# Performance work log

Measured on AMD Instinct MI355X. Metric: run time of the kernel, lower is better.

Reference implementation:

```python
import jax, jax.numpy as jnp
import numpy as np

B, M, C, D, FF, FEAT = 1, 1024, 128, 512, 1024, 20
PAIR = 3 * D + 2 * FEAT  # slow_scorer_size = 1576


def _ffnn(x, W0, b0, W1, b1):
    # FFNN(depth=1): hidden relu layer then linear output (eval mode, no dropout)
    return jax.nn.relu(x @ W0 + b0) @ W1 + b1


def _batch_gather(x, idx):
    # x: [B, M, ...], idx: [B, ...] int -> gather along mention dim per batch
    return jax.vmap(lambda xb, ib: xb[ib])(x, idx)


def _bucket_distance(d):
    # log-scale distance buckets 0..9 (identity for d<=4)
    log_idx = jnp.floor(jnp.log(jnp.maximum(d, 1).astype(jnp.float32)) / jnp.log(2.0)).astype(jnp.int32) + 3
    return jnp.clip(jnp.where(d <= 4, d, log_idx), 0, 9)


def setup_inputs() -> dict:
    key = jax.random.key(0)
    ks = jax.random.split(key, 10)
    s = 0.02
    return {
        'mention_emb': jax.random.normal(ks[0], (B, M, D), dtype=jnp.float32),
        'mention_cluster_ids': jax.random.randint(ks[1], (B, M), 0, 200),
        'mention_speaker_ids': jax.random.randint(ks[2], (B, M), 0, 2),
        'ms_W0': jax.random.normal(ks[3], (D, FF), dtype=jnp.float32) * s,
        'ms_b0': jnp.zeros((FF,), jnp.float32),
        'ms_W1': jax.random.normal(ks[4], (FF, 1), dtype=jnp.float32) * s,
        'ms_b1': jnp.zeros((1,), jnp.float32),
        'sp_W0': jax.random.normal(ks[5], (PAIR, FF), dtype=jnp.float32) * s,
        'sp_b0': jnp.zeros((FF,), jnp.float32),
        'sp_W1': jax.random.normal(ks[6], (FF, 1), dtype=jnp.float32) * s,
        'sp_b1': jnp.zeros((1,), jnp.float32),
        'speaker_emb': jax.random.normal(ks[7], (2, FEAT), dtype=jnp.float32) * s,
        'bucket_emb': jax.random.normal(ks[8], (10, FEAT), dtype=jnp.float32) * s,
    }


def reference(mention_emb, mention_cluster_ids, mention_speaker_ids,
              ms_W0, ms_b0, ms_W1, ms_b1,
              sp_W0, sp_b0, sp_W1, sp_b1,
              speaker_emb, bucket_emb):
    # mention scoring
    mention_scores = _ffnn(mention_emb, ms_W0, ms_b0, ms_W1, ms_b1)[..., 0]  # [B, M]

    # get_antecedent_info: fixed window of C previous mentions
    offsets = jnp.arange(1, C + 1)[None, None, :]                    # [1,1,C]
    raw = jnp.arange(M)[None, :, None] - offsets                      # [1,M,C]
    antecedents = jnp.broadcast_to(jnp.clip(raw, 0, M - 1), (B, M, C))
    ant_mask = jnp.broadcast_to(raw >= 0, (B, M, C))

    fast_scores = _batch_gather(mention_scores, antecedents) + mention_scores[:, :, None]
    antecedent_emb = _batch_gather(mention_emb, antecedents)          # [B,M,C,D]

    # slow pair scorer features
    same_speaker = (_batch_gather(mention_speaker_ids, antecedents) == mention_speaker_ids[:, :, None]).astype(jnp.int32)
    speaker_feat = speaker_emb[same_speaker]                          # [B,M,C,FEAT]
    bucket_feat = jnp.broadcast_to(bucket_emb[_bucket_distance(offsets)], (B, M, C, FEAT))

    src = jnp.broadcast_to(mention_emb[:, :, None, :], (B, M, C, D))
    pair_emb = jnp.concatenate([src, antecedent_emb, src * antecedent_emb, speaker_feat, bucket_feat], axis=-1)
    slow_scores = _ffnn(pair_emb, sp_W0, sp_b0, sp_W1, sp_b1)[..., 0]  # [B,M,C]

    antecedent_scores = fast_scores + slow_scores + jnp.log(ant_mask.astype(jnp.float32))
    overall_scores = jnp.concatenate([jnp.zeros((B, M, 1), jnp.float32), antecedent_scores], axis=2)
    overall_dist = jax.nn.softmax(overall_scores, axis=-1)
    eps = 1e-6
    overall_dist = jnp.clip(overall_dist, eps, 1.0 - eps)
    overall_dist = overall_dist / jnp.sum(overall_dist, axis=-1, keepdims=True)

    # coref loss from cluster ids
    ant_cluster = _batch_gather(mention_cluster_ids, antecedents) * ant_mask.astype(mention_cluster_ids.dtype)
    same_cluster = ant_cluster == mention_cluster_ids[:, :, None]
    non_dummy = (mention_cluster_ids > 0)[:, :, None]
    ant_labels = same_cluster & non_dummy
    dummy_labels = ~jnp.any(ant_labels, axis=2, keepdims=True)
    overall_labels = jnp.concatenate([dummy_labels, ant_labels], axis=2)
    loss = -jnp.sum(jnp.log(overall_dist) * overall_labels.astype(jnp.float32), axis=2)
    loss = jnp.mean(jnp.sum(loss, axis=1))
    return overall_dist, loss
```

## Files before the change

kernel.cpp:

```cpp
#include <hip/hip_runtime.h>
#include <math.h>

#define MM 1024
#define DD 512
#define CC 128
#define LDSR 516


typedef __attribute__((ext_vector_type(8))) short bf16x8;
typedef __attribute__((ext_vector_type(4), aligned(8))) short bf16x4a;
typedef __attribute__((ext_vector_type(4))) float f32x4;

__device__ __forceinline__ ushort bf16_rn(float x) {
    uint u = __float_as_uint(x);
    uint r = u + 0x7fffu + ((u >> 16) & 1u);
    return (ushort)(r >> 16);
}
__device__ __forceinline__ float bf16_to_f(ushort u) {
    return __uint_as_float(((uint)u) << 16);
}
__device__ __forceinline__ bf16x8 ld_lds16(const ushort* p) {
    bf16x4a lo = *(const bf16x4a*)p;
    bf16x4a hi = *(const bf16x4a*)(p + 4);
    return __builtin_shufflevector(lo, hi, 0, 1, 2, 3, 4, 5, 6, 7);
}

__global__ __launch_bounds__(256) void prep_all(
    const float* __restrict__ emb, ushort* __restrict__ embb,
    const float* __restrict__ ms_W0, const float* __restrict__ sp_W0,
    ushort* __restrict__ Wall, ushort* __restrict__ WfragP,
    const float* __restrict__ speaker_emb, const float* __restrict__ bucket_emb,
    float* __restrict__ spk_proj, float* __restrict__ bkt_proj)
{
    const int bid = blockIdx.x;
    const int tid = threadIdx.x;

    if (bid < 1024) {
        int i = bid * 256 + tid;
        float2 v = ((const float2*)emb)[i];
        ushort2 o;
        o.x = bf16_rn(v.x);
        o.y = bf16_rn(v.y);
        ((ushort2*)embb)[i] = o;
        return;
    }
    if (bid < 1408) {
        __shared__ float t[64][65];
        const int r = bid - 1024;
        const int k0 = (r & 7) * 64;
        const int n0 = (r >> 3) * 64;
        const int g = n0 >> 10;
        const float* src = (g == 0) ? ms_W0 : (sp_W0 + (size_t)(g - 1) * 512 * 1024);
        const int col0 = n0 & 1023;
        const int tr = tid >> 6, tc = tid & 63;
#pragma unroll
        for (int i = 0; i < 16; ++i) {
            int k = tr + i * 4;
            t[k][tc] = src[(size_t)(k0 + k) * 1024 + col0 + tc];
        }
        __syncthreads();
        const int f = tid >> 2;
        const int c4 = tid & 3;
        ushort tmp[16];
#pragma unroll
        for (int j = 0; j < 16; ++j) tmp[j] = bf16_rn(t[c4 * 16 + j][f]);
        uint4* dst = (uint4*)(Wall + (size_t)(n0 + f) * 512 + k0 + c4 * 16);
        dst[0] = *(uint4*)&tmp[0];
        dst[1] = *(uint4*)&tmp[8];
        return;
    }
    if (bid < 1664) {
        const int b4 = (bid - 1408) * 4 + (tid >> 6);
        const int l = tid & 63;
        const int g2 = b4 >> 5, s = (b4 >> 1) & 15, j = b4 & 1;
        const int wv = g2 >> 2, ft = g2 & 3;
        const int t16 = wv * 8 + ft * 2 + j;
        const int f = t16 * 16 + (l & 15);
        const int kb = s * 32 + ((l >> 4) & 3) * 8;
        const float* W = sp_W0 + (size_t)1024 * 1024;
        ushort tmp[8];
#pragma unroll
        for (int e = 0; e < 8; ++e) tmp[e] = bf16_rn(W[(size_t)(kb + e) * 1024 + f]);
        uint4* dst = (uint4*)(WfragP + (size_t)b4 * 512 + l * 8);
        *dst = *(uint4*)&tmp[0];
        return;
    }
    {
        const int r = bid - 1664;
        const float* e; const float* W; float* out;
        if (r < 2) { e = speaker_emb + r * 20; W = sp_W0 + (size_t)1536 * 1024; out = spk_proj + r * 1024; }
        else       { e = bucket_emb + (r - 2) * 20; W = sp_W0 + (size_t)1556 * 1024; out = bkt_proj + (r - 2) * 1024; }
        float ek[20];
#pragma unroll
        for (int k = 0; k < 20; ++k) ek[k] = e[k];
        for (int f = tid; f < 1024; f += 256) {
            float s = 0.f;
#pragma unroll
            for (int k = 0; k < 20; ++k) s = fmaf(ek[k], W[(size_t)k * 1024 + f], s);
            out[f] = s;
        }
        return;
    }
}

__global__ __launch_bounds__(256) void gemm_h_ms(
    const ushort* __restrict__ embb, const ushort* __restrict__ Wall,
    const float* __restrict__ ms_b0, const float* __restrict__ ms_W1,
    float* __restrict__ H, float* __restrict__ ms)
{
    const int n0 = blockIdx.x * 128;
    const int m0 = blockIdx.y * 128;
    const int lane = threadIdx.x & 63, wave = threadIdx.x >> 6;
    const int wx = wave & 1, wy = wave >> 1;
    const int l15 = lane & 15, lq = lane >> 4;

    const ushort* arow[4];
#pragma unroll
    for (int mi = 0; mi < 4; ++mi)
        arow[mi] = embb + (size_t)(m0 + wy * 64 + mi * 16 + l15) * 512;
    const ushort* brow[4];
#pragma unroll
    for (int ni = 0; ni < 4; ++ni)
        brow[ni] = Wall + (size_t)(n0 + wx * 64 + ni * 16 + l15) * 512;

    f32x4 acc[4][4];
#pragma unroll
    for (int i = 0; i < 4; ++i)
#pragma unroll
        for (int j = 0; j < 4; ++j) acc[i][j] = (f32x4)0.f;

    for (int kt = 0; kt < 512; kt += 32) {
        const int ko = kt + lq * 8;
        bf16x8 av[4], bv[4];
#pragma unroll
        for (int mi = 0; mi < 4; ++mi) av[mi] = *(const bf16x8*)(arow[mi] + ko);
#pragma unroll
        for (int ni = 0; ni < 4; ++ni) bv[ni] = *(const bf16x8*)(brow[ni] + ko);
#pragma unroll
        for (int mi = 0; mi < 4; ++mi)
#pragma unroll
            for (int ni = 0; ni < 4; ++ni)
                acc[mi][ni] = __builtin_amdgcn_mfma_f32_16x16x32_bf16(av[mi], bv[ni], acc[mi][ni], 0, 0, 0);
    }

    if (n0 < 1024) {
        float b0v[4], w1v[4];
#pragma unroll
        for (int ni = 0; ni < 4; ++ni) {
            const int col = n0 + wx * 64 + ni * 16 + l15;
            b0v[ni] = ms_b0[col];
            w1v[ni] = ms_W1[col];
        }
#pragma unroll
        for (int mi = 0; mi < 4; ++mi)
#pragma unroll
            for (int r = 0; r < 4; ++r) {
                float s = 0.f;
#pragma unroll
                for (int ni = 0; ni < 4; ++ni)
                    s += fmaxf(acc[mi][ni][r] + b0v[ni], 0.f) * w1v[ni];
                s += __shfl_xor(s, 1); s += __shfl_xor(s, 2);
                s += __shfl_xor(s, 4); s += __shfl_xor(s, 8);
                if (l15 == 0) {
                    const int mrow = m0 + wy * 64 + mi * 16 + lq * 4 + r;
                    atomicAdd(&ms[mrow], s);
                }
            }
    } else {
#pragma unroll
        for (int mi = 0; mi < 4; ++mi)
#pragma unroll
            for (int r = 0; r < 4; ++r) {
                int mrow = m0 + wy * 64 + mi * 16 + lq * 4 + r;
#pragma unroll
                for (int ni = 0; ni < 4; ++ni)
                    H[(size_t)mrow * 3072 + n0 + wx * 64 + ni * 16 + l15] = acc[mi][ni][r];
            }
    }
}

__global__ __launch_bounds__(512, 8) void pair_mfma(
    const ushort* __restrict__ embb, const ushort* __restrict__ WfragP,
    const float* __restrict__ H, const float* __restrict__ spk_proj,
    const float* __restrict__ bkt_proj, const float* __restrict__ sp_b0,
    const float* __restrict__ sp_W1, const int* __restrict__ speaker,
    float* __restrict__ slow)
{
    extern __shared__ ushort Alds[];
    float* red = (float*)(Alds + 32 * LDSR);
    int* meta_ss = (int*)(red + 8 * 32);
    int* meta_bk = meta_ss + 32;
    const int m = blockIdx.x;
    const int cq = blockIdx.y;
    const int cbase = cq * 32;
    const int tid = threadIdx.x;
    const int spk_m = speaker[m];

    {
        const int c = tid & 31;
        const int kh = (tid >> 5) * 32;
        int a = m - 1 - (cbase + c); if (a < 0) a = 0;
        const ushort* ea = embb + (size_t)a * 512 + kh;
        const ushort* em = embb + (size_t)m * 512 + kh;
        ushort* dst = Alds + c * LDSR + kh;
#pragma unroll
        for (int j = 0; j < 32; j += 8) {
            bf16x8 va = *(const bf16x8*)(ea + j);
            bf16x8 vm = *(const bf16x8*)(em + j);
            uint pr[4];
#pragma unroll
            for (int p = 0; p < 4; ++p) {
                float q0 = bf16_to_f((ushort)va[2 * p])     * bf16_to_f((ushort)vm[2 * p]);
                float q1 = bf16_to_f((ushort)va[2 * p + 1]) * bf16_to_f((ushort)vm[2 * p + 1]);
                pr[p] = __builtin_amdgcn_perm(__float_as_uint(q1), __float_as_uint(q0), 0x07060302u);
            }
            *(uint2*)(dst + j)     = *(uint2*)&pr[0];
            *(uint2*)(dst + j + 4) = *(uint2*)&pr[2];
        }
        if (tid < 32) {
            meta_ss[c] = (speaker[a] == spk_m) ? 1 : 0;
            int off = cbase + c + 1;
            int bk;
            if (off <= 4) bk = off;
            else { bk = 31 - __clz(off) + 3; if (bk > 9) bk = 9; }
            meta_bk[c] = bk;
        }
    }
    __syncthreads();

    const int lane = tid & 63;
    const int wave = __builtin_amdgcn_readfirstlane(tid >> 6);
    const int l15 = lane & 15, lq = lane >> 4;
    const ushort* ab0 = Alds + l15 * LDSR + lq * 8;

    const float* Hsrc = H + m * 3072 + 1024;
    const float* Hant = H + 2048;

    float sacc[2][4];
#pragma unroll
    for (int ct = 0; ct < 2; ++ct)
#pragma unroll
        for (int r = 0; r < 4; ++r) sacc[ct][r] = 0.f;

#pragma unroll 1
    for (int ft = 0; ft < 4; ++ft) {
        const int f0a = wave * 128 + ft * 32;
        const ushort* bb = WfragP + (size_t)(wave * 4 + ft) * 16384 + (size_t)lane * 8;
        f32x4 acc[2][2];
#pragma unroll
        for (int i = 0; i < 2; ++i)
#pragma unroll
            for (int j = 0; j < 2; ++j) acc[i][j] = (f32x4)0.f;

#pragma unroll 4
        for (int s = 0; s < 16; ++s) {
            bf16x8 b0 = *(const bf16x8*)(bb + s * 1024);
            bf16x8 b1 = *(const bf16x8*)(bb + s * 1024 + 512);
            bf16x8 a0 = ld_lds16(ab0 + s * 32);
            bf16x8 a1 = ld_lds16(ab0 + 16 * LDSR + s * 32);
            __builtin_amdgcn_s_setprio(1);
            acc[0][0] = __builtin_amdgcn_mfma_f32_16x16x32_bf16(a0, b0, acc[0][0], 0, 0, 0);
            acc[0][1] = __builtin_amdgcn_mfma_f32_16x16x32_bf16(a0, b1, acc[0][1], 0, 0, 0);
            acc[1][0] = __builtin_amdgcn_mfma_f32_16x16x32_bf16(a1, b0, acc[1][0], 0, 0, 0);
            acc[1][1] = __builtin_amdgcn_mfma_f32_16x16x32_bf16(a1, b1, acc[1][1], 0, 0, 0);
            __builtin_amdgcn_s_setprio(0);
        }

        float srcb[2], w1v[2], sp0v[2], sp1v[2];
#pragma unroll
        for (int fi = 0; fi < 2; ++fi) {
            const int fcol = f0a + fi * 16 + l15;
            srcb[fi] = Hsrc[fcol] + sp_b0[fcol];
            w1v[fi]  = sp_W1[fcol];
            sp0v[fi] = spk_proj[fcol];
            sp1v[fi] = spk_proj[1024 + fcol];
        }
#pragma unroll
        for (int ct = 0; ct < 2; ++ct) {
#pragma unroll
            for (int reg = 0; reg < 4; ++reg) {
                const int cl = ct * 16 + lq * 4 + reg;
                int a = m - 1 - (cbase + cl); if (a < 0) a = 0;
                const int ss = meta_ss[cl];
                const int aidx = a * 3072;
                const int bidx = meta_bk[cl] << 10;
                float s = sacc[ct][reg];
#pragma unroll
                for (int fi = 0; fi < 2; ++fi) {
                    const int fcol = f0a + fi * 16 + l15;
                    float bval = bkt_proj[bidx + fcol];
                    float pre = acc[ct][fi][reg] + srcb[fi] + Hant[aidx + fcol]
                              + (ss ? sp1v[fi] : sp0v[fi]) + bval;
                    s += fmaxf(pre, 0.f) * w1v[fi];
                }
                sacc[ct][reg] = s;
            }
        }
    }

#pragma unroll
    for (int ct = 0; ct < 2; ++ct) {
#pragma unroll
        for (int reg = 0; reg < 4; ++reg) {
            float s = sacc[ct][reg];
            s += __shfl_xor(s, 1); s += __shfl_xor(s, 2);
            s += __shfl_xor(s, 4); s += __shfl_xor(s, 8);
            if (l15 == 0) red[wave * 32 + ct * 16 + lq * 4 + reg] = s;
        }
    }
    __syncthreads();
    if (tid < 32) {
        float s = 0.f;
#pragma unroll
        for (int i = 0; i < 8; ++i) s += red[i * 32 + tid];
        slow[m * 128 + cbase + tid] = s;
    }
}

__device__ __forceinline__ float bsum2(float v, float* sm) {
#pragma unroll
    for (int o = 1; o < 64; o <<= 1) v += __shfl_xor(v, o);
    __syncthreads();
    if ((threadIdx.x & 63) == 0) sm[threadIdx.x >> 6] = v;
    __syncthreads();
    return sm[0] + sm[1];
}
__device__ __forceinline__ float bmax2(float v, float* sm) {
#pragma unroll
    for (int o = 1; o < 64; o <<= 1) v = fmaxf(v, __shfl_xor(v, o));
    __syncthreads();
    if ((threadIdx.x & 63) == 0) sm[threadIdx.x >> 6] = v;
    __syncthreads();
    return fmaxf(sm[0], sm[1]);
}

__global__ __launch_bounds__(128) void softmax_loss(
    const float* __restrict__ slow, const float* __restrict__ ms,
    const float* __restrict__ ms_b1,
    const float* __restrict__ sp_b1, const int* __restrict__ cluster,
    float* __restrict__ out, float* __restrict__ loss_partial)
{
    const int m = blockIdx.x, c = threadIdx.x;
    __shared__ float sm[2];
    const int raw = m - 1 - c;
    const bool maskv = raw >= 0;
    const int a = maskv ? raw : 0;
    float score = slow[(size_t)m * 128 + c] + sp_b1[0]
                + ms[m] + ms[a] + 2.f * ms_b1[0];
    if (!maskv) score = -INFINITY;

    float mx = fmaxf(bmax2(score, sm), 0.f);
    float e = expf(score - mx);
    float e0 = expf(0.f - mx);
    float sum = bsum2(e, sm) + e0;
    float p = e / sum, p0 = e0 / sum;
    const float eps = 1e-6f;
    p  = fminf(fmaxf(p,  eps), 1.f - eps);
    p0 = fminf(fmaxf(p0, eps), 1.f - eps);
    float sum2 = bsum2(p, sm) + p0;
    p /= sum2; p0 /= sum2;
    out[(size_t)m * 129 + 1 + c] = p;
    if (c == 0) out[(size_t)m * 129] = p0;

    const int cid = cluster[m];
    const bool lbl = maskv && (cid > 0) && (cluster[a] == cid);
    float anyc = bsum2(lbl ? 1.f : 0.f, sm);
    float lsum = bsum2(lbl ? -logf(p) : 0.f, sm);
    if (c == 0) {
        if (anyc == 0.f) lsum += -logf(p0);
        loss_partial[m] = lsum;
    }
}

__global__ void loss_sum(const float* __restrict__ lp, float* __restrict__ out) {
    float v = 0.f;
    for (int i = threadIdx.x; i < 1024; i += 256) v += lp[i];
#pragma unroll
    for (int o = 1; o < 64; o <<= 1) v += __shfl_xor(v, o);
    __shared__ float sm[4];
    if ((threadIdx.x & 63) == 0) sm[threadIdx.x >> 6] = v;
    __syncthreads();
    if (threadIdx.x == 0) out[(size_t)1024 * 129] = sm[0] + sm[1] + sm[2] + sm[3];
}

extern "C" void kernel_launch(void* const* d_in, const int* in_sizes, int n_in,
                              void* d_out, int out_size, void* d_ws, size_t ws_size,
                              hipStream_t stream)
{
    const float* emb   = (const float*)d_in[0];
    const int*   clus  = (const int*)  d_in[1];
    const int*   spk   = (const int*)  d_in[2];
    const float* ms_W0 = (const float*)d_in[3];
    const float* ms_b0 = (const float*)d_in[4];
    const float* ms_W1 = (const float*)d_in[5];
    const float* ms_b1 = (const float*)d_in[6];
    const float* sp_W0 = (const float*)d_in[7];
    const float* sp_b0 = (const float*)d_in[8];
    const float* sp_W1 = (const float*)d_in[9];
    const float* sp_b1 = (const float*)d_in[10];
    const float* spke  = (const float*)d_in[11];
    const float* bkte  = (const float*)d_in[12];

    float* ws = (float*)d_ws;
    float* H        = ws;
    float* slow     = ws + 3145728;
    float* spk_proj = ws + 3276800;
    float* bkt_proj = ws + 3278848;
    float* msc      = ws + 3289088;
    float* lossp    = ws + 3290112;
    ushort* embb    = (ushort*)(ws + 3291136);
    ushort* Wall    = (ushort*)(ws + 3553280);
    ushort* WfragP  = Wall + (size_t)3072 * 512;
    float* out = (float*)d_out;

    const int pair_lds = 32 * LDSR * 2 + 8 * 32 * 4 + 2 * 32 * 4;

    static bool attr_set = false;
    if (!attr_set) {
        hipFuncSetAttribute((const void*)&pair_mfma,
                            hipFuncAttributeMaxDynamicSharedMemorySize,
                            pair_lds);
        attr_set = true;
    }

    hipMemsetAsync(msc, 0, 1024 * sizeof(float), stream);
    hipLaunchKernelGGL(prep_all, dim3(1676), dim3(256), 0, stream,
                       emb, embb, ms_W0, sp_W0, Wall, WfragP,
                       spke, bkte, spk_proj, bkt_proj);
    hipLaunchKernelGGL(gemm_h_ms, dim3(24, 8), dim3(256), 0, stream,
                       embb, Wall, ms_b0, ms_W1, H, msc);
    hipLaunchKernelGGL(pair_mfma, dim3(1024, 4), dim3(512), pair_lds, stream,
                       embb, WfragP, H, spk_proj, bkt_proj, sp_b0, sp_W1, spk, slow);
    hipLaunchKernelGGL(softmax_loss, dim3(1024), dim3(128), 0, stream,
                       slow, msc, ms_b1, sp_b1, clus, out, lossp);
    hipLaunchKernelGGL(loss_sum, dim3(1), dim3(256), 0, stream, lossp, out);
}
```

Before: 329.2 us.

## Use 32x32x16 MFMA in pair kernel, shrink gemm tiles, fold memset into prep

The pair kernel now uses a single 32x32x16 bf16 MFMA per k-step instead of four 16x16x32 MFMAs, with a new weight fragment layout produced in prep and a restructured epilogue that precomputes antecedent offsets and bucket indices in LDS. The H/mention-score GEMM moves to 64x64 tiles, giving four times as many blocks to fill more CUs. The separate memset of mention scores is folded into the prep kernel, removing one launch. The aim is fewer MFMA and LDS issue slots and better occupancy, at the cost of more per-element epilogue reads and more atomics in the GEMM.

```diff
diff --git a/kernel.cpp b/kernel.cpp
--- a/kernel.cpp
+++ b/kernel.cpp
@@ -10,6 +10,7 @@
 typedef __attribute__((ext_vector_type(8))) short bf16x8;
 typedef __attribute__((ext_vector_type(4), aligned(8))) short bf16x4a;
 typedef __attribute__((ext_vector_type(4))) float f32x4;
+typedef __attribute__((ext_vector_type(16))) float f32x16;
 
 __device__ __forceinline__ ushort bf16_rn(float x) {
     uint u = __float_as_uint(x);
@@ -28,9 +29,10 @@
 __global__ __launch_bounds__(256) void prep_all(
     const float* __restrict__ emb, ushort* __restrict__ embb,
     const float* __restrict__ ms_W0, const float* __restrict__ sp_W0,
-    ushort* __restrict__ Wall, ushort* __restrict__ WfragP,
+    ushort* __restrict__ Wall, ushort* __restrict__ WfragB,
     const float* __restrict__ speaker_emb, const float* __restrict__ bucket_emb,
-    float* __restrict__ spk_proj, float* __restrict__ bkt_proj)
+    float* __restrict__ spk_proj, float* __restrict__ bkt_proj,
+    float* __restrict__ msc)
 {
     const int bid = blockIdx.x;
     const int tid = threadIdx.x;
@@ -70,23 +72,24 @@
         return;
     }
     if (bid < 1664) {
-        const int b4 = (bid - 1408) * 4 + (tid >> 6);
+        const int ts = (bid - 1408) * 4 + (tid >> 6);
         const int l = tid & 63;
-        const int g2 = b4 >> 5, s = (b4 >> 1) & 15, j = b4 & 1;
-        const int wv = g2 >> 2, ft = g2 & 3;
-        const int t16 = wv * 8 + ft * 2 + j;
-        const int f = t16 * 16 + (l & 15);
-        const int kb = s * 32 + ((l >> 4) & 3) * 8;
+        const int tt = ts >> 5, s = ts & 31;
+        const int f = tt * 32 + (l & 31);
+        const int kb = s * 16 + (l >> 5) * 8;
         const float* W = sp_W0 + (size_t)1024 * 1024;
         ushort tmp[8];
 #pragma unroll
         for (int e = 0; e < 8; ++e) tmp[e] = bf16_rn(W[(size_t)(kb + e) * 1024 + f]);
-        uint4* dst = (uint4*)(WfragP + (size_t)b4 * 512 + l * 8);
+        uint4* dst = (uint4*)(WfragB + (size_t)ts * 512 + l * 8);
         *dst = *(uint4*)&tmp[0];
         return;
     }
     {
         const int r = bid - 1664;
+        if (r == 0) {
+            for (int i = tid; i < 1024; i += 256) msc[i] = 0.f;
+        }
         const float* e; const float* W; float* out;
         if (r < 2) { e = speaker_emb + r * 20; W = sp_W0 + (size_t)1536 * 1024; out = spk_proj + r * 1024; }
         else       { e = bucket_emb + (r - 2) * 20; W = sp_W0 + (size_t)1556 * 1024; out = bkt_proj + (r - 2) * 1024; }
@@ -108,79 +111,79 @@
     const float* __restrict__ ms_b0, const float* __restrict__ ms_W1,
     float* __restrict__ H, float* __restrict__ ms)
 {
-    const int n0 = blockIdx.x * 128;
-    const int m0 = blockIdx.y * 128;
+    const int n0 = blockIdx.x * 64;
+    const int m0 = blockIdx.y * 64;
     const int lane = threadIdx.x & 63, wave = threadIdx.x >> 6;
     const int wx = wave & 1, wy = wave >> 1;
     const int l15 = lane & 15, lq = lane >> 4;
 
-    const ushort* arow[4];
-#pragma unroll
-    for (int mi = 0; mi < 4; ++mi)
-        arow[mi] = embb + (size_t)(m0 + wy * 64 + mi * 16 + l15) * 512;
-    const ushort* brow[4];
-#pragma unroll
-    for (int ni = 0; ni < 4; ++ni)
-        brow[ni] = Wall + (size_t)(n0 + wx * 64 + ni * 16 + l15) * 512;
-
-    f32x4 acc[4][4];
-#pragma unroll
-    for (int i = 0; i < 4; ++i)
-#pragma unroll
-        for (int j = 0; j < 4; ++j) acc[i][j] = (f32x4)0.f;
+    const ushort* arow[2];
+#pragma unroll
+    for (int mi = 0; mi < 2; ++mi)
+        arow[mi] = embb + (size_t)(m0 + wy * 32 + mi * 16 + l15) * 512;
+    const ushort* brow[2];
+#pragma unroll
+    for (int ni = 0; ni < 2; ++ni)
+        brow[ni] = Wall + (size_t)(n0 + wx * 32 + ni * 16 + l15) * 512;
+
+    f32x4 acc[2][2];
+#pragma unroll
+    for (int i = 0; i < 2; ++i)
+#pragma unroll
+        for (int j = 0; j < 2; ++j) acc[i][j] = (f32x4)0.f;
 
     for (int kt = 0; kt < 512; kt += 32) {
         const int ko = kt + lq * 8;
-        bf16x8 av[4], bv[4];
-#pragma unroll
-        for (int mi = 0; mi < 4; ++mi) av[mi] = *(const bf16x8*)(arow[mi] + ko);
-#pragma unroll
-        for (int ni = 0; ni < 4; ++ni) bv[ni] = *(const bf16x8*)(brow[ni] + ko);
-#pragma unroll
-        for (int mi = 0; mi < 4; ++mi)
-#pragma unroll
-            for (int ni = 0; ni < 4; ++ni)
+        bf16x8 av[2], bv[2];
+#pragma unroll
+        for (int mi = 0; mi < 2; ++mi) av[mi] = *(const bf16x8*)(arow[mi] + ko);
+#pragma unroll
+        for (int ni = 0; ni < 2; ++ni) bv[ni] = *(const bf16x8*)(brow[ni] + ko);
+#pragma unroll
+        for (int mi = 0; mi < 2; ++mi)
+#pragma unroll
+            for (int ni = 0; ni < 2; ++ni)
                 acc[mi][ni] = __builtin_amdgcn_mfma_f32_16x16x32_bf16(av[mi], bv[ni], acc[mi][ni], 0, 0, 0);
     }
 
     if (n0 < 1024) {
-        float b0v[4], w1v[4];
-#pragma unroll
-        for (int ni = 0; ni < 4; ++ni) {
-            const int col = n0 + wx * 64 + ni * 16 + l15;
+        float b0v[2], w1v[2];
+#pragma unroll
+        for (int ni = 0; ni < 2; ++ni) {
+            const int col = n0 + wx * 32 + ni * 16 + l15;
             b0v[ni] = ms_b0[col];
             w1v[ni] = ms_W1[col];
         }
 #pragma unroll
-        for (int mi = 0; mi < 4; ++mi)
+        for (int mi = 0; mi < 2; ++mi)
 #pragma unroll
             for (int r = 0; r < 4; ++r) {
                 float s = 0.f;
 #pragma unroll
-                for (int ni = 0; ni < 4; ++ni)
+                for (int ni = 0; ni < 2; ++ni)
                     s += fmaxf(acc[mi][ni][r] + b0v[ni], 0.f) * w1v[ni];
                 s += __shfl_xor(s, 1); s += __shfl_xor(s, 2);
                 s += __shfl_xor(s, 4); s += __shfl_xor(s, 8);
                 if (l15 == 0) {
-                    const int mrow = m0 + wy * 64 + mi * 16 + lq * 4 + r;
+                    const int mrow = m0 + wy * 32 + mi * 16 + lq * 4 + r;
                     atomicAdd(&ms[mrow], s);
                 }
             }
     } else {
 #pragma unroll
-        for (int mi = 0; mi < 4; ++mi)
+        for (int mi = 0; mi < 2; ++mi)
 #pragma unroll
             for (int r = 0; r < 4; ++r) {
-                int mrow = m0 + wy * 64 + mi * 16 + lq * 4 + r;
-#pragma unroll
-                for (int ni = 0; ni < 4; ++ni)
-                    H[(size_t)mrow * 3072 + n0 + wx * 64 + ni * 16 + l15] = acc[mi][ni][r];
+                int mrow = m0 + wy * 32 + mi * 16 + lq * 4 + r;
+#pragma unroll
+                for (int ni = 0; ni < 2; ++ni)
+                    H[(size_t)mrow * 3072 + n0 + wx * 32 + ni * 16 + l15] = acc[mi][ni][r];
             }
     }
 }
 
 __global__ __launch_bounds__(512, 8) void pair_mfma(
-    const ushort* __restrict__ embb, const ushort* __restrict__ WfragP,
+    const ushort* __restrict__ embb, const ushort* __restrict__ WfragB,
     const float* __restrict__ H, const float* __restrict__ spk_proj,
     const float* __restrict__ bkt_proj, const float* __restrict__ sp_b0,
     const float* __restrict__ sp_W1, const int* __restrict__ speaker,
@@ -188,8 +191,9 @@
 {
     extern __shared__ ushort Alds[];
     float* red = (float*)(Alds + 32 * LDSR);
-    int* meta_ss = (int*)(red + 8 * 32);
-    int* meta_bk = meta_ss + 32;
+    int* meta_ai = (int*)(red + 8 * 32);
+    int* meta_sb = meta_ai + 32;
+    int* meta_bi = meta_sb + 32;
     const int m = blockIdx.x;
     const int cq = blockIdx.y;
     const int cbase = cq * 32;
@@ -218,95 +222,64 @@
             *(uint2*)(dst + j + 4) = *(uint2*)&pr[2];
         }
         if (tid < 32) {
-            meta_ss[c] = (speaker[a] == spk_m) ? 1 : 0;
+            meta_sb[c] = (speaker[a] == spk_m) ? 1 : 0;
+            meta_ai[c] = a * 3072;
             int off = cbase + c + 1;
             int bk;
             if (off <= 4) bk = off;
             else { bk = 31 - __clz(off) + 3; if (bk > 9) bk = 9; }
-            meta_bk[c] = bk;
+            meta_bi[c] = bk << 10;
         }
     }
     __syncthreads();
 
     const int lane = tid & 63;
     const int wave = __builtin_amdgcn_readfirstlane(tid >> 6);
-    const int l15 = lane & 15, lq = lane >> 4;
-    const ushort* ab0 = Alds + l15 * LDSR + lq * 8;
+    const int l31 = lane & 31, k5 = lane >> 5;
+    const ushort* ab0 = Alds + l31 * LDSR + k5 * 8;
 
     const float* Hsrc = H + m * 3072 + 1024;
     const float* Hant = H + 2048;
 
-    float sacc[2][4];
-#pragma unroll
-    for (int ct = 0; ct < 2; ++ct)
-#pragma unroll
-        for (int r = 0; r < 4; ++r) sacc[ct][r] = 0.f;
+    float sacc[16];
+#pragma unroll
+    for (int r = 0; r < 16; ++r) sacc[r] = 0.f;
 
 #pragma unroll 1
     for (int ft = 0; ft < 4; ++ft) {
-        const int f0a = wave * 128 + ft * 32;
-        const ushort* bb = WfragP + (size_t)(wave * 4 + ft) * 16384 + (size_t)lane * 8;
-        f32x4 acc[2][2];
-#pragma unroll
-        for (int i = 0; i < 2; ++i)
-#pragma unroll
-            for (int j = 0; j < 2; ++j) acc[i][j] = (f32x4)0.f;
+        const ushort* bb = WfragB + (size_t)(wave * 4 + ft) * 16384 + (size_t)lane * 8;
+        f32x16 acc = (f32x16)0.f;
 
 #pragma unroll 4
-        for (int s = 0; s < 16; ++s) {
-            bf16x8 b0 = *(const bf16x8*)(bb + s * 1024);
-            bf16x8 b1 = *(const bf16x8*)(bb + s * 1024 + 512);
-            bf16x8 a0 = ld_lds16(ab0 + s * 32);
-            bf16x8 a1 = ld_lds16(ab0 + 16 * LDSR + s * 32);
+        for (int s = 0; s < 32; ++s) {
+            bf16x8 b = *(const bf16x8*)(bb + s * 512);
+            bf16x8 a = ld_lds16(ab0 + s * 16);
             __builtin_amdgcn_s_setprio(1);
-            acc[0][0] = __builtin_amdgcn_mfma_f32_16x16x32_bf16(a0, b0, acc[0][0], 0, 0, 0);
-            acc[0][1] = __builtin_amdgcn_mfma_f32_16x16x32_bf16(a0, b1, acc[0][1], 0, 0, 0);
-            acc[1][0] = __builtin_amdgcn_mfma_f32_16x16x32_bf16(a1, b0, acc[1][0], 0, 0, 0);
-            acc[1][1] = __builtin_amdgcn_mfma_f32_16x16x32_bf16(a1, b1, acc[1][1], 0, 0, 0);
+            acc = __builtin_amdgcn_mfma_f32_32x32x16_bf16(a, b, acc, 0, 0, 0);
             __builtin_amdgcn_s_setprio(0);
         }
 
-        float srcb[2], w1v[2], sp0v[2], sp1v[2];
-#pragma unroll
-        for (int fi = 0; fi < 2; ++fi) {
-            const int fcol = f0a + fi * 16 + l15;
-            srcb[fi] = Hsrc[fcol] + sp_b0[fcol];
-            w1v[fi]  = sp_W1[fcol];
-            sp0v[fi] = spk_proj[fcol];
-            sp1v[fi] = spk_proj[1024 + fcol];
-        }
-#pragma unroll
-        for (int ct = 0; ct < 2; ++ct) {
-#pragma unroll
-            for (int reg = 0; reg < 4; ++reg) {
-                const int cl = ct * 16 + lq * 4 + reg;
-                int a = m - 1 - (cbase + cl); if (a < 0) a = 0;
-                const int ss = meta_ss[cl];
-                const int aidx = a * 3072;
-                const int bidx = meta_bk[cl] << 10;
-                float s = sacc[ct][reg];
-#pragma unroll
-                for (int fi = 0; fi < 2; ++fi) {
-                    const int fcol = f0a + fi * 16 + l15;
-                    float bval = bkt_proj[bidx + fcol];
-                    float pre = acc[ct][fi][reg] + srcb[fi] + Hant[aidx + fcol]
-                              + (ss ? sp1v[fi] : sp0v[fi]) + bval;
-                    s += fmaxf(pre, 0.f) * w1v[fi];
-                }
-                sacc[ct][reg] = s;
-            }
-        }
-    }
-
-#pragma unroll
-    for (int ct = 0; ct < 2; ++ct) {
-#pragma unroll
-        for (int reg = 0; reg < 4; ++reg) {
-            float s = sacc[ct][reg];
-            s += __shfl_xor(s, 1); s += __shfl_xor(s, 2);
-            s += __shfl_xor(s, 4); s += __shfl_xor(s, 8);
-            if (l15 == 0) red[wave * 32 + ct * 16 + lq * 4 + reg] = s;
-        }
+        const int fcol = wave * 128 + ft * 32 + l31;
+        const float srcb = Hsrc[fcol] + sp_b0[fcol];
+        const float w1v  = sp_W1[fcol];
+        const float sp0  = spk_proj[fcol] + srcb;
+        const float sp1  = spk_proj[1024 + fcol] + srcb;
+#pragma unroll
+        for (int reg = 0; reg < 16; ++reg) {
+            const int cl = (reg & 3) + 8 * (reg >> 2) + 4 * k5;
+            const float spsel = meta_sb[cl] ? sp1 : sp0;
+            float pre = acc[reg] + spsel + Hant[meta_ai[cl] + fcol]
+                      + bkt_proj[meta_bi[cl] + fcol];
+            sacc[reg] += fmaxf(pre, 0.f) * w1v;
+        }
+    }
+
+#pragma unroll
+    for (int reg = 0; reg < 16; ++reg) {
+        float s = sacc[reg];
+        s += __shfl_xor(s, 1); s += __shfl_xor(s, 2);
+        s += __shfl_xor(s, 4); s += __shfl_xor(s, 8); s += __shfl_xor(s, 16);
+        if (l31 == 0) red[wave * 32 + (reg & 3) + 8 * (reg >> 2) + 4 * k5] = s;
     }
     __syncthreads();
     if (tid < 32) {
@@ -410,10 +383,10 @@
     float* lossp    = ws + 3290112;
     ushort* embb    = (ushort*)(ws + 3291136);
     ushort* Wall    = (ushort*)(ws + 3553280);
-    ushort* WfragP  = Wall + (size_t)3072 * 512;
+    ushort* WfragB  = Wall + (size_t)3072 * 512;
     float* out = (float*)d_out;
 
-    const int pair_lds = 32 * LDSR * 2 + 8 * 32 * 4 + 2 * 32 * 4;
+    const int pair_lds = 32 * LDSR * 2 + 8 * 32 * 4 + 3 * 32 * 4;
 
     static bool attr_set = false;
     if (!attr_set) {
@@ -423,14 +396,13 @@
         attr_set = true;
     }
 
-    hipMemsetAsync(msc, 0, 1024 * sizeof(float), stream);
     hipLaunchKernelGGL(prep_all, dim3(1676), dim3(256), 0, stream,
-                       emb, embb, ms_W0, sp_W0, Wall, WfragP,
-                       spke, bkte, spk_proj, bkt_proj);
-    hipLaunchKernelGGL(gemm_h_ms, dim3(24, 8), dim3(256), 0, stream,
+                       emb, embb, ms_W0, sp_W0, Wall, WfragB,
+                       spke, bkte, spk_proj, bkt_proj, msc);
+    hipLaunchKernelGGL(gemm_h_ms, dim3(48, 16), dim3(256), 0, stream,
                        embb, Wall, ms_b0, ms_W1, H, msc);
     hipLaunchKernelGGL(pair_mfma, dim3(1024, 4), dim3(512), pair_lds, stream,
-                       embb, WfragP, H, spk_proj, bkt_proj, sp_b0, sp_W1, spk, slow);
+                       embb, WfragB, H, spk_proj, bkt_proj, sp_b0, sp_W1, spk, slow);
     hipLaunchKernelGGL(softmax_loss, dim3(1024), dim3(128), 0, stream,
                        slow, msc, ms_b1, sp_b1, clus, out, lossp);
     hipLaunchKernelGGL(loss_sum, dim3(1), dim3(256), 0, stream, lossp, out);
```

After: 433.7 us. +31.8%, slower.
